# Kernel tuning notes

Hardware: AMD Instinct MI355X
Metric: run time of the kernel (lower is better)

The kernel has to match this reference:

```python
import jax, jax.numpy as jnp
import numpy as np

D_LATENT = 2048
RANK = 16

def setup_inputs() -> dict:
    key = jax.random.key(0)
    k1, k2, k3 = jax.random.split(key, 3)
    h = jax.random.normal(k1, (4, 4096, D_LATENT), dtype=jnp.float32)
    # LoRA params: original init is randn/50 for A, zeros for B; use randn/50 for
    # both so the output is non-trivial for correctness testing.
    mat_A = jax.random.normal(k2, (D_LATENT, RANK), dtype=jnp.float32) / 50.0
    mat_B = jax.random.normal(k3, (RANK, D_LATENT), dtype=jnp.float32) / 50.0
    return {"h": h, "mat_A": mat_A, "mat_B": mat_B}

def reference(h, mat_A, mat_B):
    # Faithful to torch: F.linear(h, A @ B) == h @ (A @ B).T
    W = mat_A @ mat_B                      # [d_latent, d_latent]
    return jnp.einsum('bsd,ed->bse', h, W)  # h @ W.T
```

## Files before the change

### kernel.cpp

```cpp
#include <hip/hip_runtime.h>
#include <hip/hip_bf16.h>

typedef float f4 __attribute__((ext_vector_type(4)));
typedef short bf16x8 __attribute__((ext_vector_type(8)));

#define D 2048
#define RANK 16
#define TILE 16
#define NT 512

__device__ __forceinline__ short bf16_of(float x) {
    return __builtin_bit_cast(short, __float2bfloat16(x));
}

__device__ __forceinline__ bf16x8 cvt8(f4 lo, f4 hi) {
    bf16x8 r;
    r[0] = bf16_of(lo.x); r[1] = bf16_of(lo.y);
    r[2] = bf16_of(lo.z); r[3] = bf16_of(lo.w);
    r[4] = bf16_of(hi.x); r[5] = bf16_of(hi.y);
    r[6] = bf16_of(hi.z); r[7] = bf16_of(hi.w);
    return r;
}

__device__ __forceinline__ float dot4(f4 a, f4 b) {
    return a.x * b.x + a.y * b.y + a.z * b.z + a.w * b.w;
}

__global__ __launch_bounds__(NT, 4)
void lora_mfma2(const float* __restrict__ h, const float* __restrict__ A,
                const float* __restrict__ B, float* __restrict__ out) {
    const int tid  = threadIdx.x;
    const int wave = tid >> 6;
    const int lane = tid & 63;
    const int m16  = lane & 15;
    const int kg   = lane >> 4;
    const long row0 = (long)blockIdx.x * TILE;

    __shared__ f4 ldsT[8][16][4];
    __shared__ f4 tt[16][4];

    f4 Ae[4][4];
#pragma unroll
    for (int j = 0; j < 4; ++j)
#pragma unroll
        for (int q = 0; q < 4; ++q)
            Ae[j][q] = *(const f4*)(A + (long)(tid * 4 + j) * RANK + q * 4);

    const float* pB = B + (long)m16 * D + wave * 256 + kg * 8;
    const float* ph = h + (row0 + m16) * D + wave * 256 + kg * 8;

    f4 acc = {0.f, 0.f, 0.f, 0.f};
#pragma unroll
    for (int s = 0; s < 8; ++s) {
        f4 a0 = *(const f4*)(pB + s * 32);
        f4 a1 = *(const f4*)(pB + s * 32 + 4);
        f4 b0 = *(const f4*)(ph + s * 32);
        f4 b1 = *(const f4*)(ph + s * 32 + 4);
        acc = __builtin_amdgcn_mfma_f32_16x16x32_bf16(
            cvt8(a0, a1), cvt8(b0, b1), acc, 0, 0, 0);
    }
    ldsT[wave][m16][kg] = acc;
    __syncthreads();

    if (tid < 64) {
        const int r = tid >> 2, q = tid & 3;
        f4 s = ldsT[0][r][q];
#pragma unroll
        for (int w = 1; w < 8; ++w) s += ldsT[w][r][q];
        tt[r][q] = s;
    }
    __syncthreads();

    float* po = out + row0 * D + tid * 4;
#pragma unroll
    for (int r = 0; r < TILE; ++r) {
        const f4 t0 = tt[r][0], t1 = tt[r][1], t2 = tt[r][2], t3 = tt[r][3];
        f4 res;
        res.x = dot4(t0, Ae[0][0]) + dot4(t1, Ae[0][1]) +
                dot4(t2, Ae[0][2]) + dot4(t3, Ae[0][3]);
        res.y = dot4(t0, Ae[1][0]) + dot4(t1, Ae[1][1]) +
                dot4(t2, Ae[1][2]) + dot4(t3, Ae[1][3]);
        res.z = dot4(t0, Ae[2][0]) + dot4(t1, Ae[2][1]) +
                dot4(t2, Ae[2][2]) + dot4(t3, Ae[2][3]);
        res.w = dot4(t0, Ae[3][0]) + dot4(t1, Ae[3][1]) +
                dot4(t2, Ae[3][2]) + dot4(t3, Ae[3][3]);
        __builtin_nontemporal_store(res, (f4*)(po + (long)r * D));
    }
}

extern "C" void kernel_launch(void* const* d_in, const int* in_sizes, int n_in,
                              void* d_out, int out_size, void* d_ws,
                              size_t ws_size, hipStream_t stream) {
    const float* h = (const float*)d_in[0];
    const float* A = (const float*)d_in[1];
    const float* B = (const float*)d_in[2];
    float* out = (float*)d_out;

    const int n_rows = in_sizes[0] / D;
    const int blocks = n_rows / TILE;

    hipLaunchKernelGGL(lora_mfma2, dim3(blocks), dim3(NT), 0, stream,
                       h, A, B, out);
}
```

Before: 61.76 us.

## Process two 16-row tiles per block with software-pipelined loads and B reuse

Each block now handles 32 rows as two 16-row tiles. B is converted to bf16 once and reused for both tiles. The second tile's h loads are issued before the first tile's reduction, and its MFMA overlaps the first tile's output stores. Two accumulators split the MFMA dependency chain. The barriers now wait only on LDS. The changes aim to hide global-load latency and halve the per-row B and A loads, in exchange for higher register pressure (occupancy hint lowered to 2) and half as many blocks.

```diff
diff --git a/kernel.cpp b/kernel.cpp
--- a/kernel.cpp
+++ b/kernel.cpp
@@ -6,7 +6,6 @@
 
 #define D 2048
 #define RANK 16
-#define TILE 16
 #define NT 512
 
 __device__ __forceinline__ short bf16_of(float x) {
@@ -26,65 +25,136 @@
     return a.x * b.x + a.y * b.y + a.z * b.z + a.w * b.w;
 }
 
-__global__ __launch_bounds__(NT, 4)
-void lora_mfma2(const float* __restrict__ h, const float* __restrict__ A,
-                const float* __restrict__ B, float* __restrict__ out) {
+__device__ __forceinline__ void barrier_lgkm() {
+    asm volatile("s_waitcnt lgkmcnt(0)" ::: "memory");
+    __builtin_amdgcn_s_barrier();
+}
+
+__global__ __launch_bounds__(NT, 2)
+void lora_pipe(const float* __restrict__ h, const float* __restrict__ A,
+               const float* __restrict__ B, float* __restrict__ out) {
     const int tid  = threadIdx.x;
     const int wave = tid >> 6;
     const int lane = tid & 63;
     const int m16  = lane & 15;
     const int kg   = lane >> 4;
-    const long row0 = (long)blockIdx.x * TILE;
+    const long row0 = (long)blockIdx.x * 32;
 
-    __shared__ f4 ldsT[8][16][4];
-    __shared__ f4 tt[16][4];
+    __shared__ f4 ldsT[2][8][16][4];
+    __shared__ f4 tt[2][16][4];
 
-    f4 Ae[4][4];
+    const float* pB = B + (long)m16 * D + wave * 256 + kg * 8;
+    bf16x8 Bb[8];
+#pragma unroll
+    for (int s = 0; s < 8; ++s) {
+        f4 b0 = *(const f4*)(pB + s * 32);
+        f4 b1 = *(const f4*)(pB + s * 32 + 4);
+        Bb[s] = cvt8(b0, b1);
+    }
+
+    f4 Af[4][4];
 #pragma unroll
     for (int j = 0; j < 4; ++j)
 #pragma unroll
         for (int q = 0; q < 4; ++q)
-            Ae[j][q] = *(const f4*)(A + (long)(tid * 4 + j) * RANK + q * 4);
+            Af[j][q] = *(const f4*)(A + (long)(tid * 4 + j) * RANK + q * 4);
 
-    const float* pB = B + (long)m16 * D + wave * 256 + kg * 8;
-    const float* ph = h + (row0 + m16) * D + wave * 256 + kg * 8;
+    const float* ph0 = h + (row0 + m16) * D + wave * 256 + kg * 8;
 
-    f4 acc = {0.f, 0.f, 0.f, 0.f};
+    f4 hc[16];
 #pragma unroll
     for (int s = 0; s < 8; ++s) {
-        f4 a0 = *(const f4*)(pB + s * 32);
-        f4 a1 = *(const f4*)(pB + s * 32 + 4);
-        f4 b0 = *(const f4*)(ph + s * 32);
-        f4 b1 = *(const f4*)(ph + s * 32 + 4);
-        acc = __builtin_amdgcn_mfma_f32_16x16x32_bf16(
-            cvt8(a0, a1), cvt8(b0, b1), acc, 0, 0, 0);
+        hc[2 * s]     = *(const f4*)(ph0 + s * 32);
+        hc[2 * s + 1] = *(const f4*)(ph0 + s * 32 + 4);
     }
-    ldsT[wave][m16][kg] = acc;
-    __syncthreads();
 
+    f4 a0 = {0.f, 0.f, 0.f, 0.f}, a1 = {0.f, 0.f, 0.f, 0.f};
+#pragma unroll
+    for (int s = 0; s < 4; ++s)
+        a0 = __builtin_amdgcn_mfma_f32_16x16x32_bf16(
+            Bb[s], cvt8(hc[2 * s], hc[2 * s + 1]), a0, 0, 0, 0);
+#pragma unroll
+    for (int s = 4; s < 8; ++s)
+        a1 = __builtin_amdgcn_mfma_f32_16x16x32_bf16(
+            Bb[s], cvt8(hc[2 * s], hc[2 * s + 1]), a1, 0, 0, 0);
+    ldsT[0][wave][m16][kg] = a0 + a1;
+
+    const float* ph1 = ph0 + 16 * D;
+    f4 hn[16];
+#pragma unroll
+    for (int s = 0; s < 8; ++s) {
+        hn[2 * s]     = *(const f4*)(ph1 + s * 32);
+        hn[2 * s + 1] = *(const f4*)(ph1 + s * 32 + 4);
+    }
+
+    barrier_lgkm();
     if (tid < 64) {
         const int r = tid >> 2, q = tid & 3;
-        f4 s = ldsT[0][r][q];
+        f4 s = ldsT[0][0][r][q];
 #pragma unroll
-        for (int w = 1; w < 8; ++w) s += ldsT[w][r][q];
-        tt[r][q] = s;
+        for (int w = 1; w < 8; ++w) s += ldsT[0][w][r][q];
+        tt[0][r][q] = s;
     }
-    __syncthreads();
+    barrier_lgkm();
 
-    float* po = out + row0 * D + tid * 4;
+    a0 = (f4){0.f, 0.f, 0.f, 0.f};
+    a1 = (f4){0.f, 0.f, 0.f, 0.f};
 #pragma unroll
-    for (int r = 0; r < TILE; ++r) {
-        const f4 t0 = tt[r][0], t1 = tt[r][1], t2 = tt[r][2], t3 = tt[r][3];
-        f4 res;
-        res.x = dot4(t0, Ae[0][0]) + dot4(t1, Ae[0][1]) +
-                dot4(t2, Ae[0][2]) + dot4(t3, Ae[0][3]);
-        res.y = dot4(t0, Ae[1][0]) + dot4(t1, Ae[1][1]) +
-                dot4(t2, Ae[1][2]) + dot4(t3, Ae[1][3]);
-        res.z = dot4(t0, Ae[2][0]) + dot4(t1, Ae[2][1]) +
-                dot4(t2, Ae[2][2]) + dot4(t3, Ae[2][3]);
-        res.w = dot4(t0, Ae[3][0]) + dot4(t1, Ae[3][1]) +
-                dot4(t2, Ae[3][2]) + dot4(t3, Ae[3][3]);
-        __builtin_nontemporal_store(res, (f4*)(po + (long)r * D));
+    for (int s = 0; s < 4; ++s)
+        a0 = __builtin_amdgcn_mfma_f32_16x16x32_bf16(
+            Bb[s], cvt8(hn[2 * s], hn[2 * s + 1]), a0, 0, 0, 0);
+#pragma unroll
+    for (int s = 4; s < 8; ++s)
+        a1 = __builtin_amdgcn_mfma_f32_16x16x32_bf16(
+            Bb[s], cvt8(hn[2 * s], hn[2 * s + 1]), a1, 0, 0, 0);
+    ldsT[1][wave][m16][kg] = a0 + a1;
+
+    {
+        float* po = out + row0 * D + tid * 4;
+#pragma unroll
+        for (int r = 0; r < 16; ++r) {
+            const f4 t0 = tt[0][r][0], t1 = tt[0][r][1];
+            const f4 t2 = tt[0][r][2], t3 = tt[0][r][3];
+            f4 res;
+            res.x = dot4(t0, Af[0][0]) + dot4(t1, Af[0][1]) +
+                    dot4(t2, Af[0][2]) + dot4(t3, Af[0][3]);
+            res.y = dot4(t0, Af[1][0]) + dot4(t1, Af[1][1]) +
+                    dot4(t2, Af[1][2]) + dot4(t3, Af[1][3]);
+            res.z = dot4(t0, Af[2][0]) + dot4(t1, Af[2][1]) +
+                    dot4(t2, Af[2][2]) + dot4(t3, Af[2][3]);
+            res.w = dot4(t0, Af[3][0]) + dot4(t1, Af[3][1]) +
+                    dot4(t2, Af[3][2]) + dot4(t3, Af[3][3]);
+            __builtin_nontemporal_store(res, (f4*)(po + (long)r * D));
+        }
+    }
+
+    barrier_lgkm();
+    if (tid < 64) {
+        const int r = tid >> 2, q = tid & 3;
+        f4 s = ldsT[1][0][r][q];
+#pragma unroll
+        for (int w = 1; w < 8; ++w) s += ldsT[1][w][r][q];
+        tt[1][r][q] = s;
+    }
+    barrier_lgkm();
+
+    {
+        float* po = out + (row0 + 16) * D + tid * 4;
+#pragma unroll
+        for (int r = 0; r < 16; ++r) {
+            const f4 t0 = tt[1][r][0], t1 = tt[1][r][1];
+            const f4 t2 = tt[1][r][2], t3 = tt[1][r][3];
+            f4 res;
+            res.x = dot4(t0, Af[0][0]) + dot4(t1, Af[0][1]) +
+                    dot4(t2, Af[0][2]) + dot4(t3, Af[0][3]);
+            res.y = dot4(t0, Af[1][0]) + dot4(t1, Af[1][1]) +
+                    dot4(t2, Af[1][2]) + dot4(t3, Af[1][3]);
+            res.z = dot4(t0, Af[2][0]) + dot4(t1, Af[2][1]) +
+                    dot4(t2, Af[2][2]) + dot4(t3, Af[2][3]);
+            res.w = dot4(t0, Af[3][0]) + dot4(t1, Af[3][1]) +
+                    dot4(t2, Af[3][2]) + dot4(t3, Af[3][3]);
+            __builtin_nontemporal_store(res, (f4*)(po + (long)r * D));
+        }
     }
 }
 
@@ -97,8 +167,8 @@
     float* out = (float*)d_out;
 
     const int n_rows = in_sizes[0] / D;
-    const int blocks = n_rows / TILE;
+    const int blocks = n_rows / 32;
 
-    hipLaunchKernelGGL(lora_mfma2, dim3(blocks), dim3(NT), 0, stream,
+    hipLaunchKernelGGL(lora_pipe, dim3(blocks), dim3(NT), 0, stream,
                        h, A, B, out);
 }
```

Result: slower. 67.75 us (+9.7%).

## Pack A into bf16 registers, batch h loads, split MFMA accumulator chains

Applied to the files above, without the earlier changes.

The A rows each thread holds are now stored as packed bf16 (8 registers instead of 16 floats) and widened back with shifts in the epilogue, which cuts register pressure. All B loads and all h loads are issued up front before the MFMAs, and the dependent MFMA chain is split into two independent accumulators. The barriers become an lgkmcnt wait plus s_barrier, and the output loop is unrolled by 4 only. This also rounds A to bf16, which slightly lowers epilogue precision, and the extra bf16-to-float conversions add ALU work.

```diff
diff --git a/kernel.cpp b/kernel.cpp
--- a/kernel.cpp
+++ b/kernel.cpp
@@ -6,7 +6,6 @@
 
 #define D 2048
 #define RANK 16
-#define TILE 16
 #define NT 512
 
 __device__ __forceinline__ short bf16_of(float x) {
@@ -22,46 +21,68 @@
     return r;
 }
 
-__device__ __forceinline__ float dot4(f4 a, f4 b) {
-    return a.x * b.x + a.y * b.y + a.z * b.z + a.w * b.w;
+__device__ __forceinline__ float bf2f(short s) {
+    return __uint_as_float(((unsigned)(unsigned short)s) << 16);
+}
+
+__device__ __forceinline__ void barrier_lgkm() {
+    asm volatile("s_waitcnt lgkmcnt(0)" ::: "memory");
+    __builtin_amdgcn_s_barrier();
 }
 
 __global__ __launch_bounds__(NT, 4)
-void lora_mfma2(const float* __restrict__ h, const float* __restrict__ A,
-                const float* __restrict__ B, float* __restrict__ out) {
+void lora_v7(const float* __restrict__ h, const float* __restrict__ A,
+             const float* __restrict__ B, float* __restrict__ out) {
     const int tid  = threadIdx.x;
     const int wave = tid >> 6;
     const int lane = tid & 63;
     const int m16  = lane & 15;
     const int kg   = lane >> 4;
-    const long row0 = (long)blockIdx.x * TILE;
+    const long row0 = (long)blockIdx.x * 16;
 
     __shared__ f4 ldsT[8][16][4];
     __shared__ f4 tt[16][4];
 
-    f4 Ae[4][4];
+    bf16x8 Abf[4][2];
 #pragma unroll
-    for (int j = 0; j < 4; ++j)
-#pragma unroll
-        for (int q = 0; q < 4; ++q)
-            Ae[j][q] = *(const f4*)(A + (long)(tid * 4 + j) * RANK + q * 4);
+    for (int j = 0; j < 4; ++j) {
+        const float* pa = A + (long)(tid * 4 + j) * RANK;
+        f4 a0 = *(const f4*)(pa);
+        f4 a1 = *(const f4*)(pa + 4);
+        f4 a2 = *(const f4*)(pa + 8);
+        f4 a3 = *(const f4*)(pa + 12);
+        Abf[j][0] = cvt8(a0, a1);
+        Abf[j][1] = cvt8(a2, a3);
+    }
 
     const float* pB = B + (long)m16 * D + wave * 256 + kg * 8;
-    const float* ph = h + (row0 + m16) * D + wave * 256 + kg * 8;
-
-    f4 acc = {0.f, 0.f, 0.f, 0.f};
+    bf16x8 Bb[8];
 #pragma unroll
     for (int s = 0; s < 8; ++s) {
-        f4 a0 = *(const f4*)(pB + s * 32);
-        f4 a1 = *(const f4*)(pB + s * 32 + 4);
-        f4 b0 = *(const f4*)(ph + s * 32);
-        f4 b1 = *(const f4*)(ph + s * 32 + 4);
-        acc = __builtin_amdgcn_mfma_f32_16x16x32_bf16(
-            cvt8(a0, a1), cvt8(b0, b1), acc, 0, 0, 0);
+        f4 b0 = *(const f4*)(pB + s * 32);
+        f4 b1 = *(const f4*)(pB + s * 32 + 4);
+        Bb[s] = cvt8(b0, b1);
     }
-    ldsT[wave][m16][kg] = acc;
-    __syncthreads();
 
+    const float* ph = h + (row0 + m16) * D + wave * 256 + kg * 8;
+    f4 hv[16];
+#pragma unroll
+    for (int s = 0; s < 8; ++s) {
+        hv[2 * s]     = *(const f4*)(ph + s * 32);
+        hv[2 * s + 1] = *(const f4*)(ph + s * 32 + 4);
+    }
+    f4 a0 = {0.f, 0.f, 0.f, 0.f}, a1 = {0.f, 0.f, 0.f, 0.f};
+#pragma unroll
+    for (int s = 0; s < 4; ++s)
+        a0 = __builtin_amdgcn_mfma_f32_16x16x32_bf16(
+            Bb[s], cvt8(hv[2 * s], hv[2 * s + 1]), a0, 0, 0, 0);
+#pragma unroll
+    for (int s = 4; s < 8; ++s)
+        a1 = __builtin_amdgcn_mfma_f32_16x16x32_bf16(
+            Bb[s], cvt8(hv[2 * s], hv[2 * s + 1]), a1, 0, 0, 0);
+    ldsT[wave][m16][kg] = a0 + a1;
+
+    barrier_lgkm();
     if (tid < 64) {
         const int r = tid >> 2, q = tid & 3;
         f4 s = ldsT[0][r][q];
@@ -69,21 +90,28 @@
         for (int w = 1; w < 8; ++w) s += ldsT[w][r][q];
         tt[r][q] = s;
     }
-    __syncthreads();
+    barrier_lgkm();
 
     float* po = out + row0 * D + tid * 4;
+#pragma unroll 4
+    for (int r = 0; r < 16; ++r) {
+        const f4 t0 = tt[r][0], t1 = tt[r][1];
+        const f4 t2 = tt[r][2], t3 = tt[r][3];
+        f4 res;
 #pragma unroll
-    for (int r = 0; r < TILE; ++r) {
-        const f4 t0 = tt[r][0], t1 = tt[r][1], t2 = tt[r][2], t3 = tt[r][3];
-        f4 res;
-        res.x = dot4(t0, Ae[0][0]) + dot4(t1, Ae[0][1]) +
-                dot4(t2, Ae[0][2]) + dot4(t3, Ae[0][3]);
-        res.y = dot4(t0, Ae[1][0]) + dot4(t1, Ae[1][1]) +
-                dot4(t2, Ae[1][2]) + dot4(t3, Ae[1][3]);
-        res.z = dot4(t0, Ae[2][0]) + dot4(t1, Ae[2][1]) +
-                dot4(t2, Ae[2][2]) + dot4(t3, Ae[2][3]);
-        res.w = dot4(t0, Ae[3][0]) + dot4(t1, Ae[3][1]) +
-                dot4(t2, Ae[3][2]) + dot4(t3, Ae[3][3]);
+        for (int j = 0; j < 4; ++j) {
+            const bf16x8 lo = Abf[j][0], hi = Abf[j][1];
+            float v;
+            v  = t0.x * bf2f(lo[0]) + t0.y * bf2f(lo[1]) +
+                 t0.z * bf2f(lo[2]) + t0.w * bf2f(lo[3]);
+            v += t1.x * bf2f(lo[4]) + t1.y * bf2f(lo[5]) +
+                 t1.z * bf2f(lo[6]) + t1.w * bf2f(lo[7]);
+            v += t2.x * bf2f(hi[0]) + t2.y * bf2f(hi[1]) +
+                 t2.z * bf2f(hi[2]) + t2.w * bf2f(hi[3]);
+            v += t3.x * bf2f(hi[4]) + t3.y * bf2f(hi[5]) +
+                 t3.z * bf2f(hi[6]) + t3.w * bf2f(hi[7]);
+            res[j] = v;
+        }
         __builtin_nontemporal_store(res, (f4*)(po + (long)r * D));
     }
 }
@@ -97,8 +125,8 @@
     float* out = (float*)d_out;
 
     const int n_rows = in_sizes[0] / D;
-    const int blocks = n_rows / TILE;
+    const int blocks = n_rows / 16;
 
-    hipLaunchKernelGGL(lora_mfma2, dim3(blocks), dim3(NT), 0, stream,
+    hipLaunchKernelGGL(lora_v7, dim3(blocks), dim3(NT), 0, stream,
                        h, A, B, out);
 }
```

New measurement: 64.20 us. +4.0%, slower.
